# Kernel tuning notes

Hardware: AMD Instinct MI355X
Metric: run time of the kernel (lower is better)

The kernel has to match this reference:

```python
import jax, jax.numpy as jnp
import numpy as np


def conv_transpose1d(x, w, b, stride=2, pad=1):
    # x: [B, C_in, T]; w: torch ConvTranspose1d layout [C_in, C_out, K]
    k = w.shape[-1]
    w_conv = jnp.flip(w, -1).transpose(1, 0, 2)  # [C_out, C_in, K]
    y = jax.lax.conv_general_dilated(
        x, w_conv,
        window_strides=(1,),
        padding=[(k - 1 - pad, k - 1 - pad)],
        lhs_dilation=(stride,),
        dimension_numbers=('NCH', 'OIH', 'NCH'))
    return y + b[None, :, None]


def setup_inputs() -> dict:
    key = jax.random.key(0)
    ks = jax.random.split(key, 8)
    B, T, TD, SD, HD = 8, 1024, 256, 192, 512
    C, F, TS = 3, 64, 2048  # C*F == spec_dim, TS == 2*T (cat constraint)
    return {
        'time_features': jax.random.normal(ks[0], (B, T, TD), jnp.float32),
        'spec_features': jax.random.normal(ks[1], (B, C, F, TS), jnp.float32),
        'conv_w': jax.random.normal(ks[2], (TD, TD, 4), jnp.float32) * 0.05,
        'conv_b': jnp.zeros((TD,), jnp.float32),
        'time_w': jax.random.normal(ks[3], (TD, HD), jnp.float32) * 0.05,
        'time_b': jnp.zeros((HD,), jnp.float32),
        'spec_w': jax.random.normal(ks[4], (SD, HD), jnp.float32) * 0.05,
        'spec_b': jnp.zeros((HD,), jnp.float32),
    }


def reference(time_features, spec_features, conv_w, conv_b, time_w, time_b, spec_w, spec_b):
    hd = time_w.shape[1]
    # time branch: transpose -> conv transpose (upsample x2) -> transpose back
    x = time_features.transpose(0, 2, 1)           # [B, TD, T]
    x = conv_transpose1d(x, conv_w, conv_b)        # [B, TD, 2T]
    time_feat = x.transpose(0, 2, 1)               # [B, 2T, TD]
    # spec branch: [B,C,F,Ts] -> [B,Ts,C*F]
    B, C, F, TS = spec_features.shape
    spec_feat = spec_features.transpose(0, 3, 1, 2).reshape(B, TS, C * F)
    H_time = time_feat @ time_w + time_b           # [B, 2T, HD]
    H_spec = spec_feat @ spec_w + spec_b           # [B, TS, HD]
    scale = 1.0 / jnp.sqrt(jnp.float32(hd))
    A_time = jax.nn.softmax(jnp.einsum('bth,bsh->bts', H_time, H_spec) * scale, axis=-1)
    A_spec = jax.nn.softmax(jnp.einsum('bsh,bth->bst', H_spec, H_time) * scale, axis=-1)
    fused_time = jnp.einsum('bts,bsh->bth', A_time, H_spec)  # [B, 2T, HD]
    fused_spec = jnp.einsum('bst,bth->bsh', A_spec, H_time)  # [B, TS, HD]
    return jnp.concatenate([fused_time, fused_spec], axis=-1)  # [B, 2T, 2*HD]
```

## Files before the change

### kernel.cpp

```cpp
#include <hip/hip_runtime.h>
#include <hip/hip_bf16.h>
#include <math.h>

typedef __attribute__((ext_vector_type(8))) short short8;
typedef __attribute__((ext_vector_type(4))) float f32x4;

#define BN   8
#define TSQ  2048
#define HD   512
#define TDIM 256
#define SDIM 192
#define SCALE 0.04419417382415922f

#define OFFB_G   0
#define OFFB_HB  2097152
#define OFFB_HT  4194304
#define OFFB_HS  20971520

static __device__ __forceinline__ short f2bf(float f) {
    __hip_bfloat16 h = __float2bfloat16(f);
    return *(short*)&h;
}

__global__ void k_G(const float* __restrict__ conv_w, const float* __restrict__ time_w,
                    float* __restrict__ G) {
    const int ci = blockIdx.x & 255;
    const int kk = blockIdx.x >> 8;
    const int tid = threadIdx.x;
    __shared__ float cw[256];
    cw[tid] = conv_w[(ci * 256 + tid) * 4 + kk];
    __syncthreads();
    float a0 = 0.f, a1 = 0.f;
    for (int co = 0; co < 256; ++co) {
        float w = cw[co];
        a0 += w * time_w[co * HD + tid];
        a1 += w * time_w[co * HD + tid + 256];
    }
    G[((kk * 256) + ci) * HD + tid] = a0;
    G[((kk * 256) + ci) * HD + tid + 256] = a1;
}

__global__ void k_hbias(const float* __restrict__ conv_b, const float* __restrict__ time_w,
                        const float* __restrict__ time_b, float* __restrict__ hb) {
    const int h = blockIdx.x * 256 + threadIdx.x;
    float a = time_b[h];
    for (int co = 0; co < 256; ++co) a += conv_b[co] * time_w[co * HD + h];
    hb[h] = a;
}

__global__ void k_htime(const float* __restrict__ X, const float* __restrict__ G,
                        const float* __restrict__ hb, __hip_bfloat16* __restrict__ HT) {
    const int z  = blockIdx.z;
    const int tid = threadIdx.x;
    __shared__ float As[64][21];
    __shared__ float Bs[16][68];

    const int ridx0 = blockIdx.x * 64;
    const int b  = ridx0 >> 10;
    const int m0 = ridx0 & 1023;
    const int col0 = blockIdx.y * 64;
    const int ga = z ? 2 : 1;
    const int gb = z ? 0 : 3;
    const int dm = z ? 1 : -1;

    const int lr = tid >> 2;
    const int lc = (tid & 3) * 4;
    const int bkr = tid >> 4;
    const int bc  = (tid & 15) * 4;
    const int tr = tid >> 4, tc = tid & 15;
    const int r0 = tr * 4, c0 = tc * 4;

    float acc[4][4] = {};

    for (int kk = 0; kk < 512; kk += 16) {
        {
            int k = kk + lc;
            int m = m0 + lr;
            int mm = m, ko = k;
            bool valid = true;
            if (k >= 256) { mm = m + dm; ko = k - 256; valid = (mm >= 0) && (mm < 1024); }
            float4 v = make_float4(0.f, 0.f, 0.f, 0.f);
            if (valid) v = *(const float4*)(X + ((b << 10) + mm) * TDIM + ko);
            As[lr][lc] = v.x; As[lr][lc + 1] = v.y; As[lr][lc + 2] = v.z; As[lr][lc + 3] = v.w;
        }
        {
            int k = kk + bkr;
            const float* Bp = (k < 256) ? (G + (ga * 256 + k) * HD)
                                        : (G + (gb * 256 + (k - 256)) * HD);
            float4 v = *(const float4*)(Bp + col0 + bc);
            *(float4*)&Bs[bkr][bc] = v;
        }
        __syncthreads();
#pragma unroll
        for (int kc = 0; kc < 16; ++kc) {
            float a[4], bb[4];
#pragma unroll
            for (int i = 0; i < 4; ++i) a[i] = As[r0 + i][kc];
#pragma unroll
            for (int j = 0; j < 4; ++j) bb[j] = Bs[kc][c0 + j];
#pragma unroll
            for (int i = 0; i < 4; ++i)
#pragma unroll
                for (int j = 0; j < 4; ++j) acc[i][j] += a[i] * bb[j];
        }
        __syncthreads();
    }
#pragma unroll
    for (int i = 0; i < 4; ++i) {
        int m = m0 + r0 + i;
        int t = 2 * m + z;
        __hip_bfloat16* op = HT + ((size_t)(b * TSQ) + t) * HD + col0;
#pragma unroll
        for (int j = 0; j < 4; ++j) op[c0 + j] = __float2bfloat16(acc[i][j] + hb[col0 + c0 + j]);
    }
}

__global__ void k_hspec(const float* __restrict__ S, const float* __restrict__ spec_w,
                        const float* __restrict__ spec_b, __hip_bfloat16* __restrict__ HS) {
    const int tid = threadIdx.x;
    __shared__ float As[64][21];
    __shared__ float Bs[16][68];

    const int row0 = blockIdx.x * 64;
    const int b  = row0 >> 11;
    const int t0 = row0 & 2047;
    const int col0 = blockIdx.y * 64;

    const int jc   = tid >> 4;
    const int toff = (tid & 15) * 4;
    const int tr = tid >> 4, tc = tid & 15;
    const int r0 = tr * 4, c0 = tc * 4;

    float acc[4][4] = {};

    for (int kk = 0; kk < 192; kk += 16) {
        int j = kk + jc;
        float4 v = *(const float4*)(S + ((size_t)(b * SDIM + j)) * TSQ + t0 + toff);
        As[toff][jc] = v.x; As[toff + 1][jc] = v.y; As[toff + 2][jc] = v.z; As[toff + 3][jc] = v.w;
        float4 w = *(const float4*)(spec_w + j * HD + col0 + tc * 4);
        *(float4*)&Bs[jc][tc * 4] = w;
        __syncthreads();
#pragma unroll
        for (int kc = 0; kc < 16; ++kc) {
            float a[4], bb[4];
#pragma unroll
            for (int i = 0; i < 4; ++i) a[i] = As[r0 + i][kc];
#pragma unroll
            for (int j2 = 0; j2 < 4; ++j2) bb[j2] = Bs[kc][c0 + j2];
#pragma unroll
            for (int i = 0; i < 4; ++i)
#pragma unroll
                for (int j2 = 0; j2 < 4; ++j2) acc[i][j2] += a[i] * bb[j2];
        }
        __syncthreads();
    }
#pragma unroll
    for (int i = 0; i < 4; ++i) {
        __hip_bfloat16* op = HS + ((size_t)(b * TSQ) + t0 + r0 + i) * HD + col0;
#pragma unroll
        for (int j2 = 0; j2 < 4; ++j2) op[c0 + j2] = __float2bfloat16(acc[i][j2] + spec_b[col0 + c0 + j2]);
    }
}

#define SM_K  0
#define SM_VT 32768
#define SM_P  (32768 + 40960)
#define SMEM_FLASH (32768 + 40960 + 5120)

__global__ __launch_bounds__(256)
void k_flash(const __hip_bfloat16* __restrict__ HTb, const __hip_bfloat16* __restrict__ HSb,
             float* __restrict__ out) {
    extern __shared__ char smem[];
    ushort* Kl = (ushort*)(smem + SM_K);
    ushort* Vt = (ushort*)(smem + SM_VT);
    ushort* Pl = (ushort*)(smem + SM_P);

    const int pass = blockIdx.y;
    const __hip_bfloat16* Qg = pass ? HSb : HTb;
    const __hip_bfloat16* Kg = pass ? HTb : HSb;
    const int b  = blockIdx.x & 7;
    const int qt = blockIdx.x >> 3;
    const int tid = threadIdx.x;
    const int w = tid >> 6;
    const int l = tid & 63;
    const int c = l & 15;
    const int g = l >> 4;

    ushort* Plw = Pl + w * 640;

    const __hip_bfloat16* Qrow = Qg + ((size_t)(b * TSQ) + qt * 64 + w * 16 + c) * HD;
    short8 qf[16];
#pragma unroll
    for (int kk = 0; kk < 16; ++kk) qf[kk] = *(const short8*)(Qrow + kk * 32 + g * 8);

    f32x4 acc[32];
#pragma unroll
    for (int j = 0; j < 32; ++j) acc[j] = (f32x4){0.f, 0.f, 0.f, 0.f};
    float mrow = -1e30f, lrow = 0.f;

    const __hip_bfloat16* Kb = Kg + (size_t)(b * TSQ) * HD;
    const int ss0 = (tid & 15) * 2;
    const int hb  = (tid >> 4) * 32;

    for (int s0 = 0; s0 < TSQ; s0 += 32) {
        __syncthreads();
        {
            const __hip_bfloat16* p0 = Kb + (size_t)(s0 + ss0) * HD + hb;
            const __hip_bfloat16* p1 = p0 + HD;
            short8 ra[4], rb[4];
#pragma unroll
            for (int u = 0; u < 4; ++u) { ra[u] = *(const short8*)(p0 + u * 8); rb[u] = *(const short8*)(p1 + u * 8); }
            const int sA = ss0, sB = ss0 + 1;
#pragma unroll
            for (int u = 0; u < 4; ++u) {
                *(short8*)&Kl[sA * 512 + ((hb + u * 8) ^ ((sA & 7) << 3))] = ra[u];
                *(short8*)&Kl[sB * 512 + ((hb + u * 8) ^ ((sB & 7) << 3))] = rb[u];
            }
#pragma unroll
            for (int u = 0; u < 4; ++u)
#pragma unroll
                for (int e = 0; e < 8; ++e) {
                    int i = u * 8 + e;
                    uint v = (uint)(ushort)ra[u][e] | ((uint)(ushort)rb[u][e] << 16);
                    *(uint*)&Vt[(size_t)(hb + i) * 40 + ss0] = v;
                }
        }
        __syncthreads();

        f32x4 sv[2];
#pragma unroll
        for (int st = 0; st < 2; ++st) {
            f32x4 s_ = (f32x4){0.f, 0.f, 0.f, 0.f};
            const int srow = st * 16 + c;
            const int swz = (srow & 7) << 3;
            const ushort* kp = Kl + srow * 512;
#pragma unroll
            for (int kk = 0; kk < 16; ++kk) {
                short8 kf = *(const short8*)(kp + ((kk * 32 + g * 8) ^ swz));
                s_ = __builtin_amdgcn_mfma_f32_16x16x32_bf16(kf, qf[kk], s_, 0, 0, 0);
            }
            sv[st] = s_;
        }

        float pv[8];
        float tmax = -1e30f;
#pragma unroll
        for (int st = 0; st < 2; ++st)
#pragma unroll
            for (int r = 0; r < 4; ++r) {
                float x = sv[st][r] * SCALE;
                pv[st * 4 + r] = x;
                tmax = fmaxf(tmax, x);
            }
        tmax = fmaxf(tmax, __shfl_xor(tmax, 16, 64));
        tmax = fmaxf(tmax, __shfl_xor(tmax, 32, 64));
        float mnew = fmaxf(mrow, tmax);
        float alpha = __expf(mrow - mnew);
        float tsum = 0.f;
#pragma unroll
        for (int i = 0; i < 8; ++i) { pv[i] = __expf(pv[i] - mnew); tsum += pv[i]; }
        tsum += __shfl_xor(tsum, 16, 64);
        tsum += __shfl_xor(tsum, 32, 64);
        lrow = lrow * alpha + tsum;
        mrow = mnew;

#pragma unroll
        for (int st = 0; st < 2; ++st)
#pragma unroll
            for (int pp = 0; pp < 2; ++pp) {
                int s = st * 16 + g * 4 + pp * 2;
                uint v = (uint)(ushort)f2bf(pv[st * 4 + pp * 2]) |
                         ((uint)(ushort)f2bf(pv[st * 4 + pp * 2 + 1]) << 16);
                *(uint*)&Plw[c * 40 + s] = v;
            }

#pragma unroll
        for (int r = 0; r < 4; ++r) {
            float ar = __shfl(alpha, g * 4 + r, 64);
#pragma unroll
            for (int j = 0; j < 32; ++j) acc[j][r] *= ar;
        }

        short8 pa = *(const short8*)(Plw + c * 40 + g * 8);
#pragma unroll
        for (int j = 0; j < 32; ++j) {
            short8 vb = *(const short8*)(Vt + (size_t)(j * 16 + c) * 40 + g * 8);
            acc[j] = __builtin_amdgcn_mfma_f32_16x16x32_bf16(pa, vb, acc[j], 0, 0, 0);
        }
    }

    float linv = 1.f / lrow;
    float* orow = out + ((size_t)(b * TSQ) + qt * 64 + w * 16) * 1024 + (pass ? HD : 0);
#pragma unroll
    for (int r = 0; r < 4; ++r) {
        float inv = __shfl(linv, g * 4 + r, 64);
#pragma unroll
        for (int j = 0; j < 32; ++j)
            orow[(size_t)(g * 4 + r) * 1024 + j * 16 + c] = acc[j][r] * inv;
    }
}

extern "C" void kernel_launch(void* const* d_in, const int* in_sizes, int n_in,
                              void* d_out, int out_size, void* d_ws, size_t ws_size,
                              hipStream_t stream) {
    const float* time_features = (const float*)d_in[0];
    const float* spec_features = (const float*)d_in[1];
    const float* conv_w = (const float*)d_in[2];
    const float* conv_b = (const float*)d_in[3];
    const float* time_w = (const float*)d_in[4];
    const float* time_b = (const float*)d_in[5];
    const float* spec_w = (const float*)d_in[6];
    const float* spec_b = (const float*)d_in[7];
    float* out = (float*)d_out;
    char* ws = (char*)d_ws;

    float* G  = (float*)(ws + OFFB_G);
    float* hb = (float*)(ws + OFFB_HB);
    __hip_bfloat16* HTb = (__hip_bfloat16*)(ws + OFFB_HT);
    __hip_bfloat16* HSb = (__hip_bfloat16*)(ws + OFFB_HS);

    (void)hipFuncSetAttribute((const void*)k_flash, hipFuncAttributeMaxDynamicSharedMemorySize, SMEM_FLASH);

    k_G<<<dim3(1024), 256, 0, stream>>>(conv_w, time_w, G);
    k_hbias<<<dim3(2), 256, 0, stream>>>(conv_b, time_w, time_b, hb);
    k_htime<<<dim3(128, 8, 2), 256, 0, stream>>>(time_features, G, hb, HTb);
    k_hspec<<<dim3(256, 8), 256, 0, stream>>>(spec_features, spec_w, spec_b, HSb);
    k_flash<<<dim3(256, 2), 256, SMEM_FLASH, stream>>>(HTb, HSb, out);
}
```

Baseline: 631.4 us.

## Enlarge flash blocks to 512 threads, prefetch K tiles, add lazy rescale

The flash-attention kernel now runs 8 waves per block, each handling 128 query rows, so every K/V tile staged in shared memory is shared by twice as many waves. The next K tile is loaded into registers while the current one is being consumed, and s_setprio is raised around the MFMA sections. A lazy-rescaling path skips the exp(alpha) correction and accumulator rescale when the new row max stays within 8 of the running max. The larger block increases register pressure under launch_bounds(512,2), and the skipped rescale relies on exp staying bounded, which needs care for accuracy.

```diff
diff --git a/kernel.cpp b/kernel.cpp
--- a/kernel.cpp
+++ b/kernel.cpp
@@ -3,6 +3,7 @@
 #include <math.h>
 
 typedef __attribute__((ext_vector_type(8))) short short8;
+typedef __attribute__((ext_vector_type(4))) short bf4;
 typedef __attribute__((ext_vector_type(4))) float f32x4;
 
 #define BN   8
@@ -165,9 +166,9 @@
 #define SM_K  0
 #define SM_VT 32768
 #define SM_P  (32768 + 40960)
-#define SMEM_FLASH (32768 + 40960 + 5120)
-
-__global__ __launch_bounds__(256)
+#define SMEM_FLASH (32768 + 40960 + 10240)
+
+__global__ __launch_bounds__(512, 2)
 void k_flash(const __hip_bfloat16* __restrict__ HTb, const __hip_bfloat16* __restrict__ HSb,
              float* __restrict__ out) {
     extern __shared__ char smem[];
@@ -188,7 +189,13 @@
 
     ushort* Plw = Pl + w * 640;
 
-    const __hip_bfloat16* Qrow = Qg + ((size_t)(b * TSQ) + qt * 64 + w * 16 + c) * HD;
+    const int sp = tid & 15;
+    const int sA = sp * 2, sB = sp * 2 + 1;
+    const int gg = (tid >> 4) & 3;
+    const int hbase = w * 64 + gg * 4;
+    const int swzA = (sA & 7) << 3, swzB = (sB & 7) << 3;
+
+    const __hip_bfloat16* Qrow = Qg + ((size_t)(b * TSQ) + qt * 128 + w * 16 + c) * HD;
     short8 qf[16];
 #pragma unroll
     for (int kk = 0; kk < 16; ++kk) qf[kk] = *(const short8*)(Qrow + kk * 32 + g * 8);
@@ -199,35 +206,41 @@
     float mrow = -1e30f, lrow = 0.f;
 
     const __hip_bfloat16* Kb = Kg + (size_t)(b * TSQ) * HD;
-    const int ss0 = (tid & 15) * 2;
-    const int hb  = (tid >> 4) * 32;
-
-    for (int s0 = 0; s0 < TSQ; s0 += 32) {
-        __syncthreads();
-        {
-            const __hip_bfloat16* p0 = Kb + (size_t)(s0 + ss0) * HD + hb;
-            const __hip_bfloat16* p1 = p0 + HD;
-            short8 ra[4], rb[4];
-#pragma unroll
-            for (int u = 0; u < 4; ++u) { ra[u] = *(const short8*)(p0 + u * 8); rb[u] = *(const short8*)(p1 + u * 8); }
-            const int sA = ss0, sB = ss0 + 1;
-#pragma unroll
-            for (int u = 0; u < 4; ++u) {
-                *(short8*)&Kl[sA * 512 + ((hb + u * 8) ^ ((sA & 7) << 3))] = ra[u];
-                *(short8*)&Kl[sB * 512 + ((hb + u * 8) ^ ((sB & 7) << 3))] = rb[u];
-            }
-#pragma unroll
-            for (int u = 0; u < 4; ++u)
-#pragma unroll
-                for (int e = 0; e < 8; ++e) {
-                    int i = u * 8 + e;
-                    uint v = (uint)(ushort)ra[u][e] | ((uint)(ushort)rb[u][e] << 16);
-                    *(uint*)&Vt[(size_t)(hb + i) * 40 + ss0] = v;
-                }
-        }
-        __syncthreads();
+
+    bf4 r0[4], r1[4];
+#pragma unroll
+    for (int n = 0; n < 4; ++n) {
+        r0[n] = *(const bf4*)(Kb + (size_t)sA * HD + hbase + n * 16);
+        r1[n] = *(const bf4*)(Kb + (size_t)sB * HD + hbase + n * 16);
+    }
+
+    for (int it = 0; it < 64; ++it) {
+#pragma unroll
+        for (int n = 0; n < 4; ++n) {
+            *(bf4*)&Kl[sA * 512 + ((hbase + n * 16) ^ swzA)] = r0[n];
+            *(bf4*)&Kl[sB * 512 + ((hbase + n * 16) ^ swzB)] = r1[n];
+        }
+#pragma unroll
+        for (int n = 0; n < 4; ++n)
+#pragma unroll
+            for (int m = 0; m < 4; ++m) {
+                int h = hbase + n * 16 + m;
+                uint v = (uint)(ushort)r0[n][m] | ((uint)(ushort)r1[n][m] << 16);
+                *(uint*)&Vt[h * 40 + sA] = v;
+            }
+        if (it + 1 < 64) {
+            const __hip_bfloat16* src = Kb + (size_t)((it + 1) * 32) * HD;
+#pragma unroll
+            for (int n = 0; n < 4; ++n) {
+                r0[n] = *(const bf4*)(src + (size_t)sA * HD + hbase + n * 16);
+                r1[n] = *(const bf4*)(src + (size_t)sB * HD + hbase + n * 16);
+            }
+        }
+        asm volatile("s_waitcnt lgkmcnt(0)" ::: "memory");
+        __builtin_amdgcn_s_barrier();
 
         f32x4 sv[2];
+        __builtin_amdgcn_s_setprio(1);
 #pragma unroll
         for (int st = 0; st < 2; ++st) {
             f32x4 s_ = (f32x4){0.f, 0.f, 0.f, 0.f};
@@ -241,6 +254,7 @@
             }
             sv[st] = s_;
         }
+        __builtin_amdgcn_s_setprio(0);
 
         float pv[8];
         float tmax = -1e30f;
@@ -254,15 +268,30 @@
             }
         tmax = fmaxf(tmax, __shfl_xor(tmax, 16, 64));
         tmax = fmaxf(tmax, __shfl_xor(tmax, 32, 64));
-        float mnew = fmaxf(mrow, tmax);
-        float alpha = __expf(mrow - mnew);
-        float tsum = 0.f;
-#pragma unroll
-        for (int i = 0; i < 8; ++i) { pv[i] = __expf(pv[i] - mnew); tsum += pv[i]; }
-        tsum += __shfl_xor(tsum, 16, 64);
-        tsum += __shfl_xor(tsum, 32, 64);
-        lrow = lrow * alpha + tsum;
-        mrow = mnew;
+        if (__all(tmax <= mrow + 8.0f)) {
+            float tsum = 0.f;
+#pragma unroll
+            for (int i = 0; i < 8; ++i) { pv[i] = __expf(pv[i] - mrow); tsum += pv[i]; }
+            tsum += __shfl_xor(tsum, 16, 64);
+            tsum += __shfl_xor(tsum, 32, 64);
+            lrow += tsum;
+        } else {
+            float mnew = fmaxf(mrow, tmax);
+            float alpha = __expf(mrow - mnew);
+            float tsum = 0.f;
+#pragma unroll
+            for (int i = 0; i < 8; ++i) { pv[i] = __expf(pv[i] - mnew); tsum += pv[i]; }
+            tsum += __shfl_xor(tsum, 16, 64);
+            tsum += __shfl_xor(tsum, 32, 64);
+            lrow = lrow * alpha + tsum;
+            mrow = mnew;
+#pragma unroll
+            for (int r = 0; r < 4; ++r) {
+                float ar = __shfl(alpha, g * 4 + r, 64);
+#pragma unroll
+                for (int j = 0; j < 32; ++j) acc[j][r] *= ar;
+            }
+        }
 
 #pragma unroll
         for (int st = 0; st < 2; ++st)
@@ -274,23 +303,19 @@
                 *(uint*)&Plw[c * 40 + s] = v;
             }
 
-#pragma unroll
-        for (int r = 0; r < 4; ++r) {
-            float ar = __shfl(alpha, g * 4 + r, 64);
-#pragma unroll
-            for (int j = 0; j < 32; ++j) acc[j][r] *= ar;
-        }
-
         short8 pa = *(const short8*)(Plw + c * 40 + g * 8);
+        __builtin_amdgcn_s_setprio(1);
 #pragma unroll
         for (int j = 0; j < 32; ++j) {
             short8 vb = *(const short8*)(Vt + (size_t)(j * 16 + c) * 40 + g * 8);
             acc[j] = __builtin_amdgcn_mfma_f32_16x16x32_bf16(pa, vb, acc[j], 0, 0, 0);
         }
+        __builtin_amdgcn_s_setprio(0);
+        __builtin_amdgcn_s_barrier();
     }
 
     float linv = 1.f / lrow;
-    float* orow = out + ((size_t)(b * TSQ) + qt * 64 + w * 16) * 1024 + (pass ? HD : 0);
+    float* orow = out + ((size_t)(b * TSQ) + qt * 128 + w * 16) * 1024 + (pass ? HD : 0);
 #pragma unroll
     for (int r = 0; r < 4; ++r) {
         float inv = __shfl(linv, g * 4 + r, 64);
@@ -325,5 +350,5 @@
     k_hbias<<<dim3(2), 256, 0, stream>>>(conv_b, time_w, time_b, hb);
     k_htime<<<dim3(128, 8, 2), 256, 0, stream>>>(time_features, G, hb, HTb);
     k_hspec<<<dim3(256, 8), 256, 0, stream>>>(spec_features, spec_w, spec_b, HSb);
-    k_flash<<<dim3(256, 2), 256, SMEM_FLASH, stream>>>(HTb, HSb, out);
-}
+    k_flash<<<dim3(128, 2), 512, SMEM_FLASH, stream>>>(HTb, HSb, out);
+}
```

New measurement: 1.383 ms. 119% more time.
